# Kernel tuning notes

Hardware: AMD Instinct MI355X
Metric: run time of the kernel (lower is better)

## Reference

```python
import jax, jax.numpy as jnp
import numpy as np

NX, NQ, NU, NY = 256, 64, 8, 4
N = 65536
EPS = 0.01
STD = 0.5


def setup_inputs() -> dict:
    key = jax.random.key(0)
    ks = jax.random.split(key, 8)
    return {
        "x": jax.random.normal(ks[0], (N, NX), jnp.float32),
        "u": jax.random.normal(ks[1], (N, NU), jnp.float32),
        "X": jax.random.normal(ks[2], (NX + NQ, NX + NQ), jnp.float32) * STD,
        "U": jax.random.normal(ks[3], (NX, NQ), jnp.float32) * STD,
        "Y1": jax.random.normal(ks[4], (NX, NX), jnp.float32) * STD,
        "XP": jax.random.normal(ks[5], (NX, NX), jnp.float32) * STD,
        "B2": jax.random.normal(ks[6], (NX, NU), jnp.float32) * STD,
        "D12": jax.random.normal(ks[7], (NQ, NU), jnp.float32) * STD,
        "bv": jnp.zeros((NQ,), jnp.float32),
        "t": 0,
    }


def _constrained(X, U, Y1, XP):
    # updateParameters(): build A, B1, C1, D11 from unconstrained params.
    P = XP @ XP.T + EPS * jnp.eye(NX, dtype=XP.dtype)
    H = X @ X.T + EPS * jnp.eye(NX + NQ, dtype=X.dtype)
    H11, H12, H22 = H[:NX, :NX], H[:NX, NX:], H[NX:, NX:]
    Y = -0.5 * (H11 + Y1 - Y1.T)
    Pinv = jnp.linalg.inv(P)
    A = Pinv @ Y                                   # [nx, nx]
    lam = 0.5 * jnp.diagonal(H22)                  # Lambda diagonal
    D11 = -jnp.tril(H22, -1) / lam[:, None]        # strictly lower triangular [nq, nq]
    C1 = U.T / lam[:, None]                        # [nq, nx]
    B1 = Pinv @ (-H12 - U)                         # [nx, nq]
    return A, B1, C1, D11


def _calc_w(base, D11):
    # Forward substitution: w_i = relu(base_i + sum_{j<i} D11[i,j] * w_j).
    # D11 is strictly lower triangular and unfilled w columns are zero, so a
    # full matvec against the carry is exact.
    nq = base.shape[1]

    def step(w, inp):
        i, row, b_col = inp                        # row: [nq], b_col: [Nbatch]
        wi = jax.nn.relu(b_col + w @ row)
        return w.at[:, i].set(wi), None

    w0 = jnp.zeros_like(base)
    w, _ = jax.lax.scan(step, w0, (jnp.arange(nq), D11, base.T))
    return w


def reference(x, u, X, U, Y1, XP, B2, D12, bv, t):
    A, B1, C1, D11 = _constrained(X, U, Y1, XP)
    base = x @ C1.T + u @ D12.T + bv               # [N, nq]
    w = _calc_w(base, D11)
    x_dot = x @ A.T + w @ B1.T + u @ B2.T          # [N, nx]
    return x_dot
```

## Files before the change

### kernel.cpp

```cpp
#include <hip/hip_runtime.h>

#define EPS_C 0.01f

typedef __attribute__((ext_vector_type(8))) short short8;
typedef __attribute__((ext_vector_type(4))) float f32x4;
typedef __attribute__((ext_vector_type(4))) unsigned short u16x4;
typedef __attribute__((ext_vector_type(8))) unsigned short u16x8;

#define WS_H    0
#define WS_C    102400
#define WS_C2   167936
#define WS_Y    233472
#define WS_RHS  299008
#define WS_D11  331776
#define WS_WFH  419840
#define WS_WFM  464896
#define WS_WFL  509952
#define WS_BBH  555008
#define WS_BBM  564224
#define WS_BBL  573440
#define WS_WG   582656
#define WS_E    4776960

__device__ __forceinline__ unsigned short f2bf(float f) {
    unsigned int u = __float_as_uint(f);
    unsigned int r = (u + 0x7fffu + ((u >> 16) & 1u)) >> 16;
    return (unsigned short)r;
}
__device__ __forceinline__ float bf2f(unsigned short h) {
    return __uint_as_float(((unsigned int)h) << 16);
}
__device__ __forceinline__ void split1(float f, unsigned short& h, unsigned short& m, unsigned short& l) {
    h = f2bf(f);
    float r1 = f - bf2f(h);
    m = f2bf(r1);
    l = f2bf(r1 - bf2f(m));
}
__device__ __forceinline__ void split8(const float* v, short8& h8, short8& m8, short8& l8) {
#pragma unroll
    for (int j = 0; j < 8; ++j) {
        unsigned short h, m, l;
        split1(v[j], h, m, l);
        h8[j] = (short)h; m8[j] = (short)m; l8[j] = (short)l;
    }
}

__global__ void k_build(const float* __restrict__ Xm, const float* __restrict__ XPm,
                        float* __restrict__ H, float* __restrict__ P) {
    int idx = blockIdx.x * 256 + threadIdx.x;
    if (idx < 102400) {
        int i = idx / 320, j = idx - i * 320;
        const float4* a = (const float4*)(Xm + i * 320);
        const float4* b = (const float4*)(Xm + j * 320);
        float s = 0.f;
        for (int k = 0; k < 80; ++k) {
            float4 va = a[k], vb = b[k];
            s += va.x * vb.x + va.y * vb.y + va.z * vb.z + va.w * vb.w;
        }
        H[idx] = (i == j) ? s + EPS_C : s;
    } else {
        idx -= 102400;
        if (idx < 65536) {
            int i = idx >> 8, j = idx & 255;
            const float4* a = (const float4*)(XPm + i * 256);
            const float4* b = (const float4*)(XPm + j * 256);
            float s = 0.f;
            for (int k = 0; k < 64; ++k) {
                float4 va = a[k], vb = b[k];
                s += va.x * vb.x + va.y * vb.y + va.z * vb.z + va.w * vb.w;
            }
            P[idx] = (i == j) ? s + EPS_C : s;
        }
    }
}

__global__ void k_derived(const float* __restrict__ H, const float* __restrict__ Um,
                          const float* __restrict__ Y1, const float* __restrict__ B2,
                          const float* __restrict__ D12,
                          float* __restrict__ Y, float* __restrict__ RHS,
                          float* __restrict__ D11g,
                          unsigned short* __restrict__ Bh, unsigned short* __restrict__ Bm,
                          unsigned short* __restrict__ Bl,
                          unsigned short* __restrict__ Bbh, unsigned short* __restrict__ Bbm,
                          unsigned short* __restrict__ Bbl) {
    int idx = blockIdx.x * 256 + threadIdx.x;
    if (idx < 65536) {
        int i = idx >> 8, j = idx & 255;
        Y[idx] = -0.5f * (H[i * 320 + j] + Y1[i * 256 + j] - Y1[j * 256 + i]);
        return;
    }
    idx -= 65536;
    if (idx < 16384) {
        RHS[idx] = -H[(idx >> 6) * 320 + 256 + (idx & 63)] - Um[idx];
        return;
    }
    idx -= 16384;
    if (idx < 4096) {
        int q = idx >> 6, j = idx & 63;
        float lam = 0.5f * H[(256 + q) * 320 + 256 + q];
        D11g[idx] = (j < q) ? -H[(256 + q) * 320 + 256 + j] / lam : 0.f;
        return;
    }
    idx -= 4096;
    if (idx < 8192) {
        int o = idx >> 5, cc = idx & 31;
        float f = (cc < 8) ? B2[o * 8 + cc] : 0.f;
        unsigned short h, m, l;
        split1(f, h, m, l);
        size_t off = (size_t)o * 352 + 256 + cc;
        Bh[off] = h; Bm[off] = m; Bl[off] = l;
        return;
    }
    idx -= 8192;
    if (idx < 18432) {
        int q = idx / 288, k = idx - q * 288;
        float f;
        if (k < 256) {
            float lam = 0.5f * H[(256 + q) * 320 + 256 + q];
            f = Um[(size_t)k * 64 + q] / lam;
        } else if (k < 264) f = D12[(size_t)q * 8 + (k - 256)];
        else f = 0.f;
        unsigned short h, m, l;
        split1(f, h, m, l);
        Bbh[idx] = h; Bbm[idx] = m; Bbl[idx] = l;
    }
}

__global__ void __launch_bounds__(256) k_inv8(const float* __restrict__ Cold, float* __restrict__ E, int b) {
    __shared__ __align__(16) float M[64 * 68];
    __shared__ __align__(16) float Rs[8 * 68];
    __shared__ __align__(16) float Ts[64 * 8];
    __shared__ float E8s[8 * 9];
    const int tid = threadIdx.x;
    const int ti = tid & 15, tj = tid >> 4;
#pragma unroll
    for (int t = 0; t < 4; ++t) {
        int e = tid + t * 256;
        int r = e >> 4, c4 = e & 15;
        float4 v = *(const float4*)&Cold[(size_t)(b * 64 + r) * 256 + b * 64 + c4 * 4];
        *(float4*)&M[r * 68 + c4 * 4] = v;
    }
    __syncthreads();
    for (int s = 0; s < 8; ++s) {
        if (tid < 64) {
            const int lane = tid;
            float e8[8];
#pragma unroll
            for (int j = 0; j < 8; ++j) e8[j] = 0.f;
            if (lane < 8) {
#pragma unroll
                for (int j = 0; j < 8; ++j) e8[j] = M[(s * 8 + lane) * 68 + s * 8 + j];
            }
#pragma unroll
            for (int k = 0; k < 8; ++k) {
                const float p = __shfl(e8[k], k);
                const float rinv = 1.0f / p;
                const float f = -e8[k] * rinv;
                const bool isk = (lane == k);
#pragma unroll
                for (int j = 0; j < 8; ++j) {
                    const float prj = __shfl(e8[j], k);
                    if (j == k) e8[j] = isk ? rinv : f;
                    else        e8[j] = isk ? prj * rinv : fmaf(f, prj, e8[j]);
                }
            }
            if (lane < 8) {
#pragma unroll
                for (int j = 0; j < 8; ++j) E8s[lane * 9 + j] = e8[j];
            }
        }
        __syncthreads();
#pragma unroll
        for (int t = 0; t < 2; ++t) {
            int e = tid + t * 256;
            int r = e >> 6, c = e & 63;
            Rs[r * 68 + c] = M[(s * 8 + r) * 68 + c];
        }
#pragma unroll
        for (int t = 0; t < 2; ++t) {
            int e = tid + t * 256;
            int i = e >> 3, c = e & 7;
            float acc = 0.f;
#pragma unroll
            for (int j = 0; j < 8; ++j) acc = fmaf(M[i * 68 + s * 8 + j], E8s[j * 9 + c], acc);
            Ts[i * 8 + c] = acc;
        }
        __syncthreads();
        {
            const bool rowIn = ((ti >> 1) == s);
            const bool colIn = ((tj >> 1) == s);
            const int i0 = ti * 4, j0 = tj * 4;
            float nv[4][4];
            if (rowIn && colIn) {
#pragma unroll
                for (int r = 0; r < 4; ++r)
#pragma unroll
                    for (int d = 0; d < 4; ++d)
                        nv[r][d] = E8s[(i0 - s * 8 + r) * 9 + (j0 - s * 8 + d)];
            } else if (rowIn) {
#pragma unroll
                for (int r = 0; r < 4; ++r)
#pragma unroll
                    for (int d = 0; d < 4; ++d) {
                        float acc = 0.f;
#pragma unroll
                        for (int c = 0; c < 8; ++c)
                            acc = fmaf(E8s[(i0 - s * 8 + r) * 9 + c], Rs[c * 68 + j0 + d], acc);
                        nv[r][d] = acc;
                    }
            } else if (colIn) {
#pragma unroll
                for (int r = 0; r < 4; ++r)
#pragma unroll
                    for (int d = 0; d < 4; ++d)
                        nv[r][d] = -Ts[(i0 + r) * 8 + (j0 - s * 8 + d)];
            } else {
#pragma unroll
                for (int r = 0; r < 4; ++r)
#pragma unroll
                    for (int d = 0; d < 4; ++d) {
                        float acc = M[(i0 + r) * 68 + j0 + d];
#pragma unroll
                        for (int c = 0; c < 8; ++c)
                            acc = fmaf(-Ts[(i0 + r) * 8 + c], Rs[c * 68 + j0 + d], acc);
                        nv[r][d] = acc;
                    }
            }
#pragma unroll
            for (int r = 0; r < 4; ++r)
#pragma unroll
                for (int d = 0; d < 4; ++d) M[(i0 + r) * 68 + j0 + d] = nv[r][d];
        }
        __syncthreads();
    }
#pragma unroll
    for (int t = 0; t < 4; ++t) {
        int e = tid + t * 256;
        int r = e >> 4, c4 = e & 15;
        float4 v = *(const float4*)&M[r * 68 + c4 * 4];
        *(float4*)&E[(size_t)r * 64 + c4 * 4] = v;
    }
}

__global__ void __launch_bounds__(256) k_gjS(const float* __restrict__ Cold, float* __restrict__ Cnew,
                                             float* __restrict__ E, int b, int nb) {
    const int I = blockIdx.x >> 2, J = blockIdx.x & 3;
    const int tid = threadIdx.x;
    const int ti = tid & 15, tj = tid >> 4;
    if (I == b && J == b) {
        const int r = tid >> 2, seg = tid & 3;
#pragma unroll
        for (int t = 0; t < 4; ++t) {
            float4 v = *(const float4*)&E[(size_t)r * 64 + seg * 16 + t * 4];
            *(float4*)&Cnew[(size_t)(b * 64 + r) * 256 + b * 64 + seg * 16 + t * 4] = v;
        }
        return;
    }
    __shared__ __align__(16) float Es[64 * 68];
    __shared__ __align__(16) float S1[64 * 68];
    __shared__ __align__(16) float S2[64 * 68];
    for (int e = tid; e < 1024; e += 256) {
        int r = e >> 4, c4 = e & 15;
        float4 v = *(const float4*)&E[(size_t)r * 64 + c4 * 4];
        *(float4*)&Es[r * 68 + c4 * 4] = v;
    }
    if (I == b) {
        for (int e = tid; e < 1024; e += 256) {
            int r = e >> 4, c4 = e & 15;
            float4 v = *(const float4*)&Cold[(size_t)(b * 64 + r) * 256 + J * 64 + c4 * 4];
            *(float4*)&S1[r * 68 + c4 * 4] = v;
        }
        __syncthreads();
        float acc[4][4];
#pragma unroll
        for (int r = 0; r < 4; ++r)
#pragma unroll
            for (int d = 0; d < 4; ++d) acc[r][d] = 0.f;
        for (int mm = 0; mm < 64; ++mm) {
            float a4[4], b4[4];
#pragma unroll
            for (int d = 0; d < 4; ++d) { a4[d] = Es[(ti * 4 + d) * 68 + mm]; b4[d] = S1[mm * 68 + tj * 4 + d]; }
#pragma unroll
            for (int r = 0; r < 4; ++r)
#pragma unroll
                for (int d = 0; d < 4; ++d) acc[r][d] = fmaf(a4[r], b4[d], acc[r][d]);
        }
#pragma unroll
        for (int r = 0; r < 4; ++r) {
            float4 v = {acc[r][0], acc[r][1], acc[r][2], acc[r][3]};
            *(float4*)&Cnew[(size_t)(b * 64 + ti * 4 + r) * 256 + J * 64 + tj * 4] = v;
        }
        return;
    }
    if (J == b) {
        for (int e = tid; e < 1024; e += 256) {
            int r = e >> 4, c4 = e & 15;
            float4 v = *(const float4*)&Cold[(size_t)(I * 64 + r) * 256 + b * 64 + c4 * 4];
            *(float4*)&S1[r * 68 + c4 * 4] = v;
        }
        __syncthreads();
        float acc[4][4];
#pragma unroll
        for (int r = 0; r < 4; ++r)
#pragma unroll
            for (int d = 0; d < 4; ++d) acc[r][d] = 0.f;
        for (int kk = 0; kk < 64; ++kk) {
            float a4[4], b4[4];
#pragma unroll
            for (int d = 0; d < 4; ++d) { a4[d] = S1[(ti * 4 + d) * 68 + kk]; b4[d] = Es[kk * 68 + tj * 4 + d]; }
#pragma unroll
            for (int r = 0; r < 4; ++r)
#pragma unroll
                for (int d = 0; d < 4; ++d) acc[r][d] = fmaf(a4[r], b4[d], acc[r][d]);
        }
#pragma unroll
        for (int r = 0; r < 4; ++r) {
            float4 v = {-acc[r][0], -acc[r][1], -acc[r][2], -acc[r][3]};
            *(float4*)&Cnew[(size_t)(I * 64 + ti * 4 + r) * 256 + b * 64 + tj * 4] = v;
        }
        return;
    }
    for (int e = tid; e < 1024; e += 256) {
        int r = e >> 4, c4 = e & 15;
        float4 v = *(const float4*)&Cold[(size_t)(I * 64 + r) * 256 + b * 64 + c4 * 4];
        *(float4*)&S1[r * 68 + c4 * 4] = v;
        float4 w = *(const float4*)&Cold[(size_t)(b * 64 + r) * 256 + J * 64 + c4 * 4];
        *(float4*)&S2[r * 68 + c4 * 4] = w;
    }
    __syncthreads();
    float t4[4][4];
#pragma unroll
    for (int r = 0; r < 4; ++r)
#pragma unroll
        for (int d = 0; d < 4; ++d) t4[r][d] = 0.f;
    for (int kk = 0; kk < 64; ++kk) {
        float a4[4], b4[4];
#pragma unroll
        for (int d = 0; d < 4; ++d) { a4[d] = S1[(ti * 4 + d) * 68 + kk]; b4[d] = Es[kk * 68 + tj * 4 + d]; }
#pragma unroll
        for (int r = 0; r < 4; ++r)
#pragma unroll
            for (int d = 0; d < 4; ++d) t4[r][d] = fmaf(a4[r], b4[d], t4[r][d]);
    }
    __syncthreads();
#pragma unroll
    for (int r = 0; r < 4; ++r)
#pragma unroll
        for (int d = 0; d < 4; ++d) S1[(ti * 4 + r) * 68 + tj * 4 + d] = t4[r][d];
    __syncthreads();
    float acc[4][4];
#pragma unroll
    for (int r = 0; r < 4; ++r) {
        float4 cv = *(const float4*)&Cold[(size_t)(I * 64 + ti * 4 + r) * 256 + J * 64 + tj * 4];
        acc[r][0] = cv.x; acc[r][1] = cv.y; acc[r][2] = cv.z; acc[r][3] = cv.w;
    }
    for (int kk = 0; kk < 64; ++kk) {
        float a4[4], b4[4];
#pragma unroll
        for (int d = 0; d < 4; ++d) { a4[d] = S1[(ti * 4 + d) * 68 + kk]; b4[d] = S2[kk * 68 + tj * 4 + d]; }
#pragma unroll
        for (int r = 0; r < 4; ++r)
#pragma unroll
            for (int d = 0; d < 4; ++d) acc[r][d] = fmaf(-a4[r], b4[d], acc[r][d]);
    }
#pragma unroll
    for (int r = 0; r < 4; ++r) {
        float4 v = {acc[r][0], acc[r][1], acc[r][2], acc[r][3]};
        *(float4*)&Cnew[(size_t)(I * 64 + ti * 4 + r) * 256 + J * 64 + tj * 4] = v;
    }
    if (I == nb && J == nb) {
        float* M   = Es;
        float* Rs2 = S2;
        float* Ts2 = S2 + 1024;
        float* E8s = S2 + 1664;
        __syncthreads();
#pragma unroll
        for (int r = 0; r < 4; ++r)
#pragma unroll
            for (int d = 0; d < 4; ++d)
                M[(ti * 4 + r) * 68 + tj * 4 + d] = acc[r][d];
        __syncthreads();
        for (int s = 0; s < 8; ++s) {
            if (tid < 64) {
                const int lane = tid;
                float e8[8];
#pragma unroll
                for (int j = 0; j < 8; ++j) e8[j] = 0.f;
                if (lane < 8) {
#pragma unroll
                    for (int j = 0; j < 8; ++j) e8[j] = M[(s * 8 + lane) * 68 + s * 8 + j];
                }
#pragma unroll
                for (int k = 0; k < 8; ++k) {
                    const float p = __shfl(e8[k], k);
                    const float rinv = 1.0f / p;
                    const float f = -e8[k] * rinv;
                    const bool isk = (lane == k);
#pragma unroll
                    for (int j = 0; j < 8; ++j) {
                        const float prj = __shfl(e8[j], k);
                        if (j == k) e8[j] = isk ? rinv : f;
                        else        e8[j] = isk ? prj * rinv : fmaf(f, prj, e8[j]);
                    }
                }
                if (lane < 8) {
#pragma unroll
                    for (int j = 0; j < 8; ++j) E8s[lane * 9 + j] = e8[j];
                }
            }
            __syncthreads();
#pragma unroll
            for (int t = 0; t < 2; ++t) {
                int e = tid + t * 256;
                int r = e >> 6, c = e & 63;
                Rs2[r * 68 + c] = M[(s * 8 + r) * 68 + c];
            }
#pragma unroll
            for (int t = 0; t < 2; ++t) {
                int e = tid + t * 256;
                int i = e >> 3, c = e & 7;
                float a2 = 0.f;
#pragma unroll
                for (int j = 0; j < 8; ++j) a2 = fmaf(M[i * 68 + s * 8 + j], E8s[j * 9 + c], a2);
                Ts2[i * 8 + c] = a2;
            }
            __syncthreads();
            {
                const bool rowIn = ((ti >> 1) == s);
                const bool colIn = ((tj >> 1) == s);
                const int i0 = ti * 4, j0 = tj * 4;
                float nv[4][4];
                if (rowIn && colIn) {
#pragma unroll
                    for (int r = 0; r < 4; ++r)
#pragma unroll
                        for (int d = 0; d < 4; ++d)
                            nv[r][d] = E8s[(i0 - s * 8 + r) * 9 + (j0 - s * 8 + d)];
                } else if (rowIn) {
#pragma unroll
                    for (int r = 0; r < 4; ++r)
#pragma unroll
                        for (int d = 0; d < 4; ++d) {
                            float a2 = 0.f;
#pragma unroll
                            for (int c = 0; c < 8; ++c)
                                a2 = fmaf(E8s[(i0 - s * 8 + r) * 9 + c], Rs2[c * 68 + j0 + d], a2);
                            nv[r][d] = a2;
                        }
                } else if (colIn) {
#pragma unroll
                    for (int r = 0; r < 4; ++r)
#pragma unroll
                        for (int d = 0; d < 4; ++d)
                            nv[r][d] = -Ts2[(i0 + r) * 8 + (j0 - s * 8 + d)];
                } else {
#pragma unroll
                    for (int r = 0; r < 4; ++r)
#pragma unroll
                        for (int d = 0; d < 4; ++d) {
                            float a2 = M[(i0 + r) * 68 + j0 + d];
#pragma unroll
                            for (int c = 0; c < 8; ++c)
                                a2 = fmaf(-Ts2[(i0 + r) * 8 + c], Rs2[c * 68 + j0 + d], a2);
                            nv[r][d] = a2;
                        }
                }
#pragma unroll
                for (int r = 0; r < 4; ++r)
#pragma unroll
                    for (int d = 0; d < 4; ++d) M[(i0 + r) * 68 + j0 + d] = nv[r][d];
            }
            __syncthreads();
        }
#pragma unroll
        for (int t = 0; t < 4; ++t) {
            int e = tid + t * 256;
            int r = e >> 4, c4 = e & 15;
            float4 v = *(const float4*)&M[r * 68 + c4 * 4];
            *(float4*)&E[(size_t)r * 64 + c4 * 4] = v;
        }
    }
}

__global__ void __launch_bounds__(256) k_apply2(const float* __restrict__ PI, const float* __restrict__ Y,
                                                const float* __restrict__ RHS,
                                                unsigned short* __restrict__ Bh, unsigned short* __restrict__ Bm,
                                                unsigned short* __restrict__ Bl) {
    const int i0 = ((int)blockIdx.x / 5) * 64;
    const int c0 = ((int)blockIdx.x % 5) * 64;
    __shared__ __align__(16) float S1[64 * 68], S2[64 * 68];
    const int tid = threadIdx.x;
    const int ti = tid & 15, tj = tid >> 4;
    float acc[4][4];
#pragma unroll
    for (int r = 0; r < 4; ++r)
#pragma unroll
        for (int d = 0; d < 4; ++d) acc[r][d] = 0.f;
    for (int kc = 0; kc < 4; ++kc) {
        __syncthreads();
        for (int e = tid; e < 1024; e += 256) {
            int i = e >> 4, k4 = e & 15;
            float4 v = *(const float4*)&PI[(size_t)(i0 + i) * 256 + kc * 64 + k4 * 4];
            S1[(k4 * 4 + 0) * 68 + i] = v.x;
            S1[(k4 * 4 + 1) * 68 + i] = v.y;
            S1[(k4 * 4 + 2) * 68 + i] = v.z;
            S1[(k4 * 4 + 3) * 68 + i] = v.w;
            float4 w;
            if (c0 < 256) w = *(const float4*)&Y[(size_t)(kc * 64 + i) * 256 + c0 + k4 * 4];
            else          w = *(const float4*)&RHS[(size_t)(kc * 64 + i) * 64 + k4 * 4];
            *(float4*)&S2[i * 68 + k4 * 4] = w;
        }
        __syncthreads();
        for (int kk = 0; kk < 64; ++kk) {
            float4 pv = *(const float4*)&S1[kk * 68 + ti * 4];
            float4 gv = *(const float4*)&S2[kk * 68 + tj * 4];
            float p4[4] = {pv.x, pv.y, pv.z, pv.w};
            float g4[4] = {gv.x, gv.y, gv.z, gv.w};
#pragma unroll
            for (int r = 0; r < 4; ++r)
#pragma unroll
                for (int d = 0; d < 4; ++d) acc[r][d] = fmaf(p4[r], g4[d], acc[r][d]);
        }
    }
    const int pc0 = (c0 < 256) ? c0 : 288;
#pragma unroll
    for (int r = 0; r < 4; ++r)
#pragma unroll
        for (int d = 0; d < 4; ++d) {
            unsigned short h, m, l;
            split1(acc[r][d], h, m, l);
            size_t off = (size_t)(i0 + ti * 4 + r) * 352 + pc0 + tj * 4 + d;
            Bh[off] = h; Bm[off] = m; Bl[off] = l;
        }
}

#define XSTR 264
__global__ void __launch_bounds__(256, 3) k_base(const float* __restrict__ x, const float* __restrict__ u,
                                                 const unsigned short* __restrict__ Bbh,
                                                 const unsigned short* __restrict__ Bbm,
                                                 const unsigned short* __restrict__ Bbl,
                                                 const float* __restrict__ bv,
                                                 float* __restrict__ wg) {
    __shared__ __align__(16) unsigned short Ah[32 * XSTR];
    __shared__ __align__(16) unsigned short Am[32 * XSTR];
    __shared__ __align__(16) unsigned short Al[32 * XSTR];
    const int tid = threadIdx.x;
    const int r0 = blockIdx.x * 32;
    {
        const float4* xg4 = (const float4*)(x + (size_t)r0 * 256);
#pragma unroll
        for (int i = 0; i < 8; ++i) {
            int e = tid + i * 256, r = e >> 6, c4 = e & 63;
            float4 v = xg4[e];
            float vv[4] = {v.x, v.y, v.z, v.w};
            u16x4 hv, mv, lv;
#pragma unroll
            for (int j = 0; j < 4; ++j) {
                unsigned short h, m, l;
                split1(vv[j], h, m, l);
                hv[j] = h; mv[j] = m; lv[j] = l;
            }
            *(u16x4*)&Ah[r * XSTR + c4 * 4] = hv;
            *(u16x4*)&Am[r * XSTR + c4 * 4] = mv;
            *(u16x4*)&Al[r * XSTR + c4 * 4] = lv;
        }
    }
    __syncthreads();
    const int lane = tid & 63, wid = tid >> 6;
    const int n0 = wid * 16;
    const int lr = lane & 15, lg = lane >> 4;
    const int lk = lg * 8;
    const int noff = (n0 + lr) * 288;
    f32x4 acc[2];
    acc[0] = (f32x4){0.f, 0.f, 0.f, 0.f};
    acc[1] = (f32x4){0.f, 0.f, 0.f, 0.f};
    short8 cb_h, nb_h, b_m, b_l;
    cb_h = *(const short8*)&Bbh[noff + lk];
#pragma unroll
    for (int kt = 0; kt < 9; ++kt) {
        const int ka = kt * 32 + lk;
        b_m = *(const short8*)&Bbm[noff + ka];
        b_l = *(const short8*)&Bbl[noff + ka];
        if (kt < 8) nb_h = *(const short8*)&Bbh[noff + ka + 32];
        short8 a_h[2], a_m[2], a_l[2];
        if (kt < 8) {
            a_h[0] = *(const short8*)&Ah[lr * XSTR + ka];
            a_h[1] = *(const short8*)&Ah[(16 + lr) * XSTR + ka];
            a_m[0] = *(const short8*)&Am[lr * XSTR + ka];
            a_m[1] = *(const short8*)&Am[(16 + lr) * XSTR + ka];
            a_l[0] = *(const short8*)&Al[lr * XSTR + ka];
            a_l[1] = *(const short8*)&Al[(16 + lr) * XSTR + ka];
        } else {
            if (lg == 0) {
                float vv[8];
                const float4* up = (const float4*)&u[(size_t)(r0 + lr) * 8];
                float4 v0 = up[0], v1 = up[1];
                vv[0] = v0.x; vv[1] = v0.y; vv[2] = v0.z; vv[3] = v0.w;
                vv[4] = v1.x; vv[5] = v1.y; vv[6] = v1.z; vv[7] = v1.w;
                split8(vv, a_h[0], a_m[0], a_l[0]);
                const float4* up2 = (const float4*)&u[(size_t)(r0 + 16 + lr) * 8];
                float4 w0 = up2[0], w1 = up2[1];
                vv[0] = w0.x; vv[1] = w0.y; vv[2] = w0.z; vv[3] = w0.w;
                vv[4] = w1.x; vv[5] = w1.y; vv[6] = w1.z; vv[7] = w1.w;
                split8(vv, a_h[1], a_m[1], a_l[1]);
            } else {
                short8 z = {0, 0, 0, 0, 0, 0, 0, 0};
                a_h[0] = z; a_h[1] = z; a_m[0] = z; a_m[1] = z; a_l[0] = z; a_l[1] = z;
            }
        }
#pragma unroll
        for (int m = 0; m < 2; ++m) {
            acc[m] = __builtin_amdgcn_mfma_f32_16x16x32_bf16(a_h[m], cb_h, acc[m], 0, 0, 0);
            acc[m] = __builtin_amdgcn_mfma_f32_16x16x32_bf16(a_m[m], cb_h, acc[m], 0, 0, 0);
            acc[m] = __builtin_amdgcn_mfma_f32_16x16x32_bf16(a_l[m], cb_h, acc[m], 0, 0, 0);
        }
#pragma unroll
        for (int m = 0; m < 2; ++m) {
            acc[m] = __builtin_amdgcn_mfma_f32_16x16x32_bf16(a_h[m], b_m, acc[m], 0, 0, 0);
            acc[m] = __builtin_amdgcn_mfma_f32_16x16x32_bf16(a_m[m], b_m, acc[m], 0, 0, 0);
        }
#pragma unroll
        for (int m = 0; m < 2; ++m)
            acc[m] = __builtin_amdgcn_mfma_f32_16x16x32_bf16(a_h[m], b_l, acc[m], 0, 0, 0);
        if (kt < 8) cb_h = nb_h;
    }
    const float bvv = bv[n0 + lr];
#pragma unroll
    for (int m = 0; m < 2; ++m)
#pragma unroll
        for (int j = 0; j < 4; ++j)
            wg[(size_t)(r0 + m * 16 + lg * 4 + j) * 64 + n0 + lr] = acc[m][j] + bvv;
}

__global__ void __launch_bounds__(256) k_rec(float* __restrict__ wg, const float* __restrict__ D11g) {
    __shared__ float D[64 * 64];
    const int tid = threadIdx.x;
#pragma unroll
    for (int t = 0; t < 16; ++t) D[tid + t * 256] = D11g[tid + t * 256];
    __syncthreads();
    const size_t r = (size_t)blockIdx.x * 256 + tid;
    float w[64];
    float* wr = wg + r * 64;
#pragma unroll
    for (int c = 0; c < 16; ++c) {
        float4 v = *(const float4*)&wr[c * 4];
        w[4 * c] = v.x; w[4 * c + 1] = v.y; w[4 * c + 2] = v.z; w[4 * c + 3] = v.w;
    }
    w[0] = fmaxf(w[0], 0.f);
#pragma unroll
    for (int i = 1; i < 64; ++i) {
        float s0 = w[i], s1 = 0.f, s2 = 0.f, s3 = 0.f;
#pragma unroll
        for (int j = 0; j + 3 < i; j += 4) {
            s0 = fmaf(w[j + 0], D[i * 64 + j + 0], s0);
            s1 = fmaf(w[j + 1], D[i * 64 + j + 1], s1);
            s2 = fmaf(w[j + 2], D[i * 64 + j + 2], s2);
            s3 = fmaf(w[j + 3], D[i * 64 + j + 3], s3);
        }
#pragma unroll
        for (int j = i & ~3; j < i; ++j) s0 = fmaf(w[j], D[i * 64 + j], s0);
        w[i] = fmaxf((s0 + s1) + (s2 + s3), 0.f);
    }
#pragma unroll
    for (int c = 0; c < 16; ++c) {
        float4 v = {w[4 * c], w[4 * c + 1], w[4 * c + 2], w[4 * c + 3]};
        *(float4*)&wr[c * 4] = v;
    }
}

__global__ void __launch_bounds__(256, 3) k_m2(const float* __restrict__ x, const float* __restrict__ wg,
                                               const float* __restrict__ u,
                                               const unsigned short* __restrict__ Bh,
                                               const unsigned short* __restrict__ Bm,
                                               const unsigned short* __restrict__ Bl,
                                               float* __restrict__ out) {
    __shared__ __align__(16) unsigned short Ah[32 * XSTR];
    __shared__ __align__(16) unsigned short Am[32 * XSTR];
    __shared__ __align__(16) unsigned short Al[32 * XSTR];
    const int tid = threadIdx.x;
    const int r0 = blockIdx.x * 32;
    {
        const float4* xg4 = (const float4*)(x + (size_t)r0 * 256);
#pragma unroll
        for (int i = 0; i < 8; ++i) {
            int e = tid + i * 256, r = e >> 6, c4 = e & 63;
            float4 v = xg4[e];
            float vv[4] = {v.x, v.y, v.z, v.w};
            u16x4 hv, mv, lv;
#pragma unroll
            for (int j = 0; j < 4; ++j) {
                unsigned short h, m, l;
                split1(vv[j], h, m, l);
                hv[j] = h; mv[j] = m; lv[j] = l;
            }
            *(u16x4*)&Ah[r * XSTR + c4 * 4] = hv;
            *(u16x4*)&Am[r * XSTR + c4 * 4] = mv;
            *(u16x4*)&Al[r * XSTR + c4 * 4] = lv;
        }
    }
    __syncthreads();
    const int lane = tid & 63, wid = tid >> 6;
    const int n0 = wid * 64;
    const int lr = lane & 15, lg = lane >> 4;
    const int lk = lg * 8;
    int noff[4];
#pragma unroll
    for (int nf = 0; nf < 4; ++nf) noff[nf] = (n0 + nf * 16 + lr) * 352;
    f32x4 acc[2][4];
#pragma unroll
    for (int m = 0; m < 2; ++m)
#pragma unroll
        for (int nf = 0; nf < 4; ++nf) acc[m][nf] = (f32x4){0.f, 0.f, 0.f, 0.f};
    short8 cb_h[4], nb_h[4], b_m[4], b_l[4];
#pragma unroll
    for (int nf = 0; nf < 4; ++nf) cb_h[nf] = *(const short8*)&Bh[noff[nf] + lk];
#pragma unroll
    for (int kt = 0; kt < 11; ++kt) {
        const int ka = kt * 32 + lk;
#pragma unroll
        for (int nf = 0; nf < 4; ++nf) b_m[nf] = *(const short8*)&Bm[noff[nf] + ka];
#pragma unroll
        for (int nf = 0; nf < 4; ++nf) b_l[nf] = *(const short8*)&Bl[noff[nf] + ka];
        if (kt < 10) {
#pragma unroll
            for (int nf = 0; nf < 4; ++nf) nb_h[nf] = *(const short8*)&Bh[noff[nf] + ka + 32];
        }
        short8 a_h[2], a_m[2], a_l[2];
        if (kt < 8) {
            a_h[0] = *(const short8*)&Ah[lr * XSTR + ka];
            a_h[1] = *(const short8*)&Ah[(16 + lr) * XSTR + ka];
            a_m[0] = *(const short8*)&Am[lr * XSTR + ka];
            a_m[1] = *(const short8*)&Am[(16 + lr) * XSTR + ka];
            a_l[0] = *(const short8*)&Al[lr * XSTR + ka];
            a_l[1] = *(const short8*)&Al[(16 + lr) * XSTR + ka];
        } else if (kt == 8) {
            if (lg == 0) {
                float vv[8];
                const float4* up = (const float4*)&u[(size_t)(r0 + lr) * 8];
                float4 v0 = up[0], v1 = up[1];
                vv[0] = v0.x; vv[1] = v0.y; vv[2] = v0.z; vv[3] = v0.w;
                vv[4] = v1.x; vv[5] = v1.y; vv[6] = v1.z; vv[7] = v1.w;
                split8(vv, a_h[0], a_m[0], a_l[0]);
                const float4* up2 = (const float4*)&u[(size_t)(r0 + 16 + lr) * 8];
                float4 w0 = up2[0], w1 = up2[1];
                vv[0] = w0.x; vv[1] = w0.y; vv[2] = w0.z; vv[3] = w0.w;
                vv[4] = w1.x; vv[5] = w1.y; vv[6] = w1.z; vv[7] = w1.w;
                split8(vv, a_h[1], a_m[1], a_l[1]);
            } else {
                short8 z = {0, 0, 0, 0, 0, 0, 0, 0};
                a_h[0] = z; a_h[1] = z; a_m[0] = z; a_m[1] = z; a_l[0] = z; a_l[1] = z;
            }
        } else {
            const int wc = (kt - 9) * 32 + lk;
            float vv[8];
            const float4* wp = (const float4*)&wg[(size_t)(r0 + lr) * 64 + wc];
            float4 v0 = wp[0], v1 = wp[1];
            vv[0] = v0.x; vv[1] = v0.y; vv[2] = v0.z; vv[3] = v0.w;
            vv[4] = v1.x; vv[5] = v1.y; vv[6] = v1.z; vv[7] = v1.w;
            split8(vv, a_h[0], a_m[0], a_l[0]);
            const float4* wp2 = (const float4*)&wg[(size_t)(r0 + 16 + lr) * 64 + wc];
            float4 w0 = wp2[0], w1 = wp2[1];
            vv[0] = w0.x; vv[1] = w0.y; vv[2] = w0.z; vv[3] = w0.w;
            vv[4] = w1.x; vv[5] = w1.y; vv[6] = w1.z; vv[7] = w1.w;
            split8(vv, a_h[1], a_m[1], a_l[1]);
        }
#pragma unroll
        for (int nf = 0; nf < 4; ++nf)
#pragma unroll
            for (int m = 0; m < 2; ++m) {
                acc[m][nf] = __builtin_amdgcn_mfma_f32_16x16x32_bf16(a_h[m], cb_h[nf], acc[m][nf], 0, 0, 0);
                acc[m][nf] = __builtin_amdgcn_mfma_f32_16x16x32_bf16(a_m[m], cb_h[nf], acc[m][nf], 0, 0, 0);
                acc[m][nf] = __builtin_amdgcn_mfma_f32_16x16x32_bf16(a_l[m], cb_h[nf], acc[m][nf], 0, 0, 0);
            }
#pragma unroll
        for (int nf = 0; nf < 4; ++nf)
#pragma unroll
            for (int m = 0; m < 2; ++m) {
                acc[m][nf] = __builtin_amdgcn_mfma_f32_16x16x32_bf16(a_h[m], b_m[nf], acc[m][nf], 0, 0, 0);
                acc[m][nf] = __builtin_amdgcn_mfma_f32_16x16x32_bf16(a_m[m], b_m[nf], acc[m][nf], 0, 0, 0);
                if (kt >= 9)
                    acc[m][nf] = __builtin_amdgcn_mfma_f32_16x16x32_bf16(a_l[m], b_m[nf], acc[m][nf], 0, 0, 0);
            }
#pragma unroll
        for (int nf = 0; nf < 4; ++nf)
#pragma unroll
            for (int m = 0; m < 2; ++m) {
                acc[m][nf] = __builtin_amdgcn_mfma_f32_16x16x32_bf16(a_h[m], b_l[nf], acc[m][nf], 0, 0, 0);
                if (kt >= 9)
                    acc[m][nf] = __builtin_amdgcn_mfma_f32_16x16x32_bf16(a_m[m], b_l[nf], acc[m][nf], 0, 0, 0);
            }
        if (kt < 10) {
#pragma unroll
            for (int nf = 0; nf < 4; ++nf) cb_h[nf] = nb_h[nf];
        }
    }
#pragma unroll
    for (int m = 0; m < 2; ++m)
#pragma unroll
        for (int nf = 0; nf < 4; ++nf)
#pragma unroll
            for (int j = 0; j < 4; ++j)
                out[(size_t)(r0 + m * 16 + lg * 4 + j) * 256 + n0 + nf * 16 + lr] = acc[m][nf][j];
}

extern "C" void kernel_launch(void* const* d_in, const int* in_sizes, int n_in,
                              void* d_out, int out_size, void* d_ws, size_t ws_size,
                              hipStream_t stream) {
    const float* x   = (const float*)d_in[0];
    const float* u   = (const float*)d_in[1];
    const float* Xm  = (const float*)d_in[2];
    const float* Um  = (const float*)d_in[3];
    const float* Y1  = (const float*)d_in[4];
    const float* XPm = (const float*)d_in[5];
    const float* B2  = (const float*)d_in[6];
    const float* D12 = (const float*)d_in[7];
    const float* bv  = (const float*)d_in[8];
    float* out = (float*)d_out;
    float* ws  = (float*)d_ws;

    float* H    = ws + WS_H;
    float* C0   = ws + WS_C;
    float* C1   = ws + WS_C2;
    float* Y    = ws + WS_Y;
    float* RHS  = ws + WS_RHS;
    float* D11g = ws + WS_D11;
    float* E    = ws + WS_E;
    unsigned short* Bh  = (unsigned short*)(ws + WS_WFH);
    unsigned short* Bm  = (unsigned short*)(ws + WS_WFM);
    unsigned short* Bl  = (unsigned short*)(ws + WS_WFL);
    unsigned short* Bbh = (unsigned short*)(ws + WS_BBH);
    unsigned short* Bbm = (unsigned short*)(ws + WS_BBM);
    unsigned short* Bbl = (unsigned short*)(ws + WS_BBL);
    float* wg = ws + WS_WG;

    k_build<<<656, 256, 0, stream>>>(Xm, XPm, H, C0);
    k_derived<<<441, 256, 0, stream>>>(H, Um, Y1, B2, D12, Y, RHS, D11g,
                                       Bh, Bm, Bl, Bbh, Bbm, Bbl);
    k_base<<<2048, 256, 0, stream>>>(x, u, Bbh, Bbm, Bbl, bv, wg);
    k_rec<<<256, 256, 0, stream>>>(wg, D11g);
    k_inv8<<<1, 256, 0, stream>>>(C0, E, 0);
    k_gjS<<<16, 256, 0, stream>>>(C0, C1, E, 0, 1);
    k_gjS<<<16, 256, 0, stream>>>(C1, C0, E, 1, 2);
    k_gjS<<<16, 256, 0, stream>>>(C0, C1, E, 2, 3);
    k_gjS<<<16, 256, 0, stream>>>(C1, C0, E, 3, -1);
    k_apply2<<<20, 256, 0, stream>>>(C0, Y, RHS, Bh, Bm, Bl);
    k_m2<<<2048, 256, 0, stream>>>(x, wg, u, Bh, Bm, Bl, out);
}
```

Baseline: 373.6 us.

## Fuse base GEMM, recurrence and output GEMM into one kernel

Merges k_base, k_rec and k_m2 into a single k_main kernel. Each block keeps its 32 rows of split x in LDS and reuses them for both GEMMs, holds the base/w tile in shared memory, and runs the triangular recurrence cooperatively with 8 lanes per row and shuffle reductions. This removes the global round trip of the wg buffer, two launches, and the second load and split of x. In exchange, occupancy drops (launch bounds 3 to 2, more LDS), the B-operand prefetch pipelining is dropped, and the recurrence becomes 64 serial steps per block with only 32 of the rows active in parallel.

```diff
diff --git a/kernel.cpp b/kernel.cpp
--- a/kernel.cpp
+++ b/kernel.cpp
@@ -19,8 +19,7 @@
 #define WS_BBH  555008
 #define WS_BBM  564224
 #define WS_BBL  573440
-#define WS_WG   582656
-#define WS_E    4776960
+#define WS_E    582656
 
 __device__ __forceinline__ unsigned short f2bf(float f) {
     unsigned int u = __float_as_uint(f);
@@ -535,15 +534,21 @@
 }
 
 #define XSTR 264
-__global__ void __launch_bounds__(256, 3) k_base(const float* __restrict__ x, const float* __restrict__ u,
+__global__ void __launch_bounds__(256, 2) k_main(const float* __restrict__ x, const float* __restrict__ u,
                                                  const unsigned short* __restrict__ Bbh,
                                                  const unsigned short* __restrict__ Bbm,
                                                  const unsigned short* __restrict__ Bbl,
                                                  const float* __restrict__ bv,
-                                                 float* __restrict__ wg) {
+                                                 const float* __restrict__ D11g,
+                                                 const unsigned short* __restrict__ Bh,
+                                                 const unsigned short* __restrict__ Bm,
+                                                 const unsigned short* __restrict__ Bl,
+                                                 float* __restrict__ out) {
     __shared__ __align__(16) unsigned short Ah[32 * XSTR];
     __shared__ __align__(16) unsigned short Am[32 * XSTR];
     __shared__ __align__(16) unsigned short Al[32 * XSTR];
+    __shared__ __align__(16) float bs[32 * 68];
+    __shared__ __align__(16) float D11s[64 * 64];
     const int tid = threadIdx.x;
     const int r0 = blockIdx.x * 32;
     {
@@ -564,234 +569,191 @@
             *(u16x4*)&Am[r * XSTR + c4 * 4] = mv;
             *(u16x4*)&Al[r * XSTR + c4 * 4] = lv;
         }
+#pragma unroll
+        for (int t = 0; t < 16; ++t) D11s[tid + t * 256] = D11g[tid + t * 256];
     }
     __syncthreads();
     const int lane = tid & 63, wid = tid >> 6;
-    const int n0 = wid * 16;
     const int lr = lane & 15, lg = lane >> 4;
     const int lk = lg * 8;
-    const int noff = (n0 + lr) * 288;
-    f32x4 acc[2];
-    acc[0] = (f32x4){0.f, 0.f, 0.f, 0.f};
-    acc[1] = (f32x4){0.f, 0.f, 0.f, 0.f};
-    short8 cb_h, nb_h, b_m, b_l;
-    cb_h = *(const short8*)&Bbh[noff + lk];
-#pragma unroll
-    for (int kt = 0; kt < 9; ++kt) {
+    {
+        const int n0 = wid * 16;
+        const int noff = (n0 + lr) * 288;
+        f32x4 acc[2];
+        acc[0] = (f32x4){0.f, 0.f, 0.f, 0.f};
+        acc[1] = (f32x4){0.f, 0.f, 0.f, 0.f};
+        for (int kt = 0; kt < 9; ++kt) {
+            const int ka = kt * 32 + lk;
+            short8 a_h[2], a_m[2], a_l[2];
+            if (kt < 8) {
+                a_h[0] = *(const short8*)&Ah[lr * XSTR + ka];
+                a_h[1] = *(const short8*)&Ah[(16 + lr) * XSTR + ka];
+                a_m[0] = *(const short8*)&Am[lr * XSTR + ka];
+                a_m[1] = *(const short8*)&Am[(16 + lr) * XSTR + ka];
+                a_l[0] = *(const short8*)&Al[lr * XSTR + ka];
+                a_l[1] = *(const short8*)&Al[(16 + lr) * XSTR + ka];
+            } else {
+                if (lg == 0) {
+                    float vv[8];
+                    const float4* up = (const float4*)&u[(size_t)(r0 + lr) * 8];
+                    float4 v0 = up[0], v1 = up[1];
+                    vv[0] = v0.x; vv[1] = v0.y; vv[2] = v0.z; vv[3] = v0.w;
+                    vv[4] = v1.x; vv[5] = v1.y; vv[6] = v1.z; vv[7] = v1.w;
+                    split8(vv, a_h[0], a_m[0], a_l[0]);
+                    const float4* up2 = (const float4*)&u[(size_t)(r0 + 16 + lr) * 8];
+                    float4 w0 = up2[0], w1 = up2[1];
+                    vv[0] = w0.x; vv[1] = w0.y; vv[2] = w0.z; vv[3] = w0.w;
+                    vv[4] = w1.x; vv[5] = w1.y; vv[6] = w1.z; vv[7] = w1.w;
+                    split8(vv, a_h[1], a_m[1], a_l[1]);
+                } else {
+                    short8 z = {0, 0, 0, 0, 0, 0, 0, 0};
+                    a_h[0] = z; a_h[1] = z; a_m[0] = z; a_m[1] = z; a_l[0] = z; a_l[1] = z;
+                }
+            }
+            short8 b_h = *(const short8*)&Bbh[noff + ka];
+            short8 b_m = *(const short8*)&Bbm[noff + ka];
+            short8 b_l = *(const short8*)&Bbl[noff + ka];
+#pragma unroll
+            for (int m = 0; m < 2; ++m) {
+                acc[m] = __builtin_amdgcn_mfma_f32_16x16x32_bf16(a_h[m], b_h, acc[m], 0, 0, 0);
+                acc[m] = __builtin_amdgcn_mfma_f32_16x16x32_bf16(a_m[m], b_h, acc[m], 0, 0, 0);
+                acc[m] = __builtin_amdgcn_mfma_f32_16x16x32_bf16(a_h[m], b_m, acc[m], 0, 0, 0);
+                acc[m] = __builtin_amdgcn_mfma_f32_16x16x32_bf16(a_l[m], b_h, acc[m], 0, 0, 0);
+                acc[m] = __builtin_amdgcn_mfma_f32_16x16x32_bf16(a_m[m], b_m, acc[m], 0, 0, 0);
+                acc[m] = __builtin_amdgcn_mfma_f32_16x16x32_bf16(a_h[m], b_l, acc[m], 0, 0, 0);
+            }
+        }
+        const float bvv = bv[n0 + lr];
+#pragma unroll
+        for (int m = 0; m < 2; ++m)
+#pragma unroll
+            for (int j = 0; j < 4; ++j)
+                bs[(m * 16 + lg * 4 + j) * 68 + n0 + lr] = acc[m][j] + bvv;
+    }
+    __syncthreads();
+    {
+        const int p = tid & 7, rr = tid >> 3;
+        float* wrow = bs + rr * 68;
+        for (int i = 0; i < 64; ++i) {
+            float s = 0.f;
+            for (int j = p; j < i; j += 8) s = fmaf(wrow[j], D11s[i * 64 + j], s);
+            s += __shfl_xor(s, 1);
+            s += __shfl_xor(s, 2);
+            s += __shfl_xor(s, 4);
+            if (p == 0) {
+                const float wi = wrow[i] + s;
+                wrow[i] = wi > 0.f ? wi : 0.f;
+            }
+        }
+    }
+    __syncthreads();
+    const int n0 = wid * 64;
+    f32x4 acc[2][4];
+#pragma unroll
+    for (int m = 0; m < 2; ++m)
+#pragma unroll
+        for (int nf = 0; nf < 4; ++nf) acc[m][nf] = (f32x4){0.f, 0.f, 0.f, 0.f};
+
+#define M2_MFMA6()                                                                               \
+    for (int nf = 0; nf < 4; ++nf) {                                                             \
+        for (int m = 0; m < 2; ++m) {                                                            \
+            acc[m][nf] = __builtin_amdgcn_mfma_f32_16x16x32_bf16(a_h[m], b_h[nf], acc[m][nf], 0, 0, 0); \
+            acc[m][nf] = __builtin_amdgcn_mfma_f32_16x16x32_bf16(a_m[m], b_h[nf], acc[m][nf], 0, 0, 0); \
+            acc[m][nf] = __builtin_amdgcn_mfma_f32_16x16x32_bf16(a_h[m], b_m[nf], acc[m][nf], 0, 0, 0); \
+            acc[m][nf] = __builtin_amdgcn_mfma_f32_16x16x32_bf16(a_l[m], b_h[nf], acc[m][nf], 0, 0, 0); \
+            acc[m][nf] = __builtin_amdgcn_mfma_f32_16x16x32_bf16(a_m[m], b_m[nf], acc[m][nf], 0, 0, 0); \
+            acc[m][nf] = __builtin_amdgcn_mfma_f32_16x16x32_bf16(a_h[m], b_l[nf], acc[m][nf], 0, 0, 0); \
+        }                                                                                        \
+    }
+
+    for (int kt = 0; kt < 8; ++kt) {
         const int ka = kt * 32 + lk;
-        b_m = *(const short8*)&Bbm[noff + ka];
-        b_l = *(const short8*)&Bbl[noff + ka];
-        if (kt < 8) nb_h = *(const short8*)&Bbh[noff + ka + 32];
         short8 a_h[2], a_m[2], a_l[2];
-        if (kt < 8) {
-            a_h[0] = *(const short8*)&Ah[lr * XSTR + ka];
-            a_h[1] = *(const short8*)&Ah[(16 + lr) * XSTR + ka];
-            a_m[0] = *(const short8*)&Am[lr * XSTR + ka];
-            a_m[1] = *(const short8*)&Am[(16 + lr) * XSTR + ka];
-            a_l[0] = *(const short8*)&Al[lr * XSTR + ka];
-            a_l[1] = *(const short8*)&Al[(16 + lr) * XSTR + ka];
+        a_h[0] = *(const short8*)&Ah[lr * XSTR + ka];
+        a_h[1] = *(const short8*)&Ah[(16 + lr) * XSTR + ka];
+        a_m[0] = *(const short8*)&Am[lr * XSTR + ka];
+        a_m[1] = *(const short8*)&Am[(16 + lr) * XSTR + ka];
+        a_l[0] = *(const short8*)&Al[lr * XSTR + ka];
+        a_l[1] = *(const short8*)&Al[(16 + lr) * XSTR + ka];
+        short8 b_h[4], b_m[4], b_l[4];
+#pragma unroll
+        for (int nf = 0; nf < 4; ++nf) {
+            const size_t n = (size_t)(n0 + nf * 16 + lr);
+            b_h[nf] = *(const short8*)&Bh[n * 352 + ka];
+            b_m[nf] = *(const short8*)&Bm[n * 352 + ka];
+            b_l[nf] = *(const short8*)&Bl[n * 352 + ka];
+        }
+#pragma unroll
+        M2_MFMA6()
+    }
+    {
+        const int ka = 256 + lk;
+        short8 a_h[2], a_m[2], a_l[2];
+        if (lg == 0) {
+            float vv[8];
+            const float4* up = (const float4*)&u[(size_t)(r0 + lr) * 8];
+            float4 v0 = up[0], v1 = up[1];
+            vv[0] = v0.x; vv[1] = v0.y; vv[2] = v0.z; vv[3] = v0.w;
+            vv[4] = v1.x; vv[5] = v1.y; vv[6] = v1.z; vv[7] = v1.w;
+            split8(vv, a_h[0], a_m[0], a_l[0]);
+            const float4* up2 = (const float4*)&u[(size_t)(r0 + 16 + lr) * 8];
+            float4 w0 = up2[0], w1 = up2[1];
+            vv[0] = w0.x; vv[1] = w0.y; vv[2] = w0.z; vv[3] = w0.w;
+            vv[4] = w1.x; vv[5] = w1.y; vv[6] = w1.z; vv[7] = w1.w;
+            split8(vv, a_h[1], a_m[1], a_l[1]);
         } else {
-            if (lg == 0) {
-                float vv[8];
-                const float4* up = (const float4*)&u[(size_t)(r0 + lr) * 8];
-                float4 v0 = up[0], v1 = up[1];
-                vv[0] = v0.x; vv[1] = v0.y; vv[2] = v0.z; vv[3] = v0.w;
-                vv[4] = v1.x; vv[5] = v1.y; vv[6] = v1.z; vv[7] = v1.w;
-                split8(vv, a_h[0], a_m[0], a_l[0]);
-                const float4* up2 = (const float4*)&u[(size_t)(r0 + 16 + lr) * 8];
-                float4 w0 = up2[0], w1 = up2[1];
-                vv[0] = w0.x; vv[1] = w0.y; vv[2] = w0.z; vv[3] = w0.w;
-                vv[4] = w1.x; vv[5] = w1.y; vv[6] = w1.z; vv[7] = w1.w;
-                split8(vv, a_h[1], a_m[1], a_l[1]);
-            } else {
-                short8 z = {0, 0, 0, 0, 0, 0, 0, 0};
-                a_h[0] = z; a_h[1] = z; a_m[0] = z; a_m[1] = z; a_l[0] = z; a_l[1] = z;
-            }
-        }
-#pragma unroll
-        for (int m = 0; m < 2; ++m) {
-            acc[m] = __builtin_amdgcn_mfma_f32_16x16x32_bf16(a_h[m], cb_h, acc[m], 0, 0, 0);
-            acc[m] = __builtin_amdgcn_mfma_f32_16x16x32_bf16(a_m[m], cb_h, acc[m], 0, 0, 0);
-            acc[m] = __builtin_amdgcn_mfma_f32_16x16x32_bf16(a_l[m], cb_h, acc[m], 0, 0, 0);
-        }
-#pragma unroll
-        for (int m = 0; m < 2; ++m) {
-            acc[m] = __builtin_amdgcn_mfma_f32_16x16x32_bf16(a_h[m], b_m, acc[m], 0, 0, 0);
-            acc[m] = __builtin_amdgcn_mfma_f32_16x16x32_bf16(a_m[m], b_m, acc[m], 0, 0, 0);
-        }
-#pragma unroll
-        for (int m = 0; m < 2; ++m)
-            acc[m] = __builtin_amdgcn_mfma_f32_16x16x32_bf16(a_h[m], b_l, acc[m], 0, 0, 0);
-        if (kt < 8) cb_h = nb_h;
-    }
-    const float bvv = bv[n0 + lr];
-#pragma unroll
-    for (int m = 0; m < 2; ++m)
-#pragma unroll
-        for (int j = 0; j < 4; ++j)
-            wg[(size_t)(r0 + m * 16 + lg * 4 + j) * 64 + n0 + lr] = acc[m][j] + bvv;
-}
-
-__global__ void __launch_bounds__(256) k_rec(float* __restrict__ wg, const float* __restrict__ D11g) {
-    __shared__ float D[64 * 64];
-    const int tid = threadIdx.x;
-#pragma unroll
-    for (int t = 0; t < 16; ++t) D[tid + t * 256] = D11g[tid + t * 256];
-    __syncthreads();
-    const size_t r = (size_t)blockIdx.x * 256 + tid;
-    float w[64];
-    float* wr = wg + r * 64;
-#pragma unroll
-    for (int c = 0; c < 16; ++c) {
-        float4 v = *(const float4*)&wr[c * 4];
-        w[4 * c] = v.x; w[4 * c + 1] = v.y; w[4 * c + 2] = v.z; w[4 * c + 3] = v.w;
-    }
-    w[0] = fmaxf(w[0], 0.f);
-#pragma unroll
-    for (int i = 1; i < 64; ++i) {
-        float s0 = w[i], s1 = 0.f, s2 = 0.f, s3 = 0.f;
-#pragma unroll
-        for (int j = 0; j + 3 < i; j += 4) {
-            s0 = fmaf(w[j + 0], D[i * 64 + j + 0], s0);
-            s1 = fmaf(w[j + 1], D[i * 64 + j + 1], s1);
-            s2 = fmaf(w[j + 2], D[i * 64 + j + 2], s2);
-            s3 = fmaf(w[j + 3], D[i * 64 + j + 3], s3);
-        }
-#pragma unroll
-        for (int j = i & ~3; j < i; ++j) s0 = fmaf(w[j], D[i * 64 + j], s0);
-        w[i] = fmaxf((s0 + s1) + (s2 + s3), 0.f);
-    }
-#pragma unroll
-    for (int c = 0; c < 16; ++c) {
-        float4 v = {w[4 * c], w[4 * c + 1], w[4 * c + 2], w[4 * c + 3]};
-        *(float4*)&wr[c * 4] = v;
-    }
-}
-
-__global__ void __launch_bounds__(256, 3) k_m2(const float* __restrict__ x, const float* __restrict__ wg,
-                                               const float* __restrict__ u,
-                                               const unsigned short* __restrict__ Bh,
-                                               const unsigned short* __restrict__ Bm,
-                                               const unsigned short* __restrict__ Bl,
-                                               float* __restrict__ out) {
-    __shared__ __align__(16) unsigned short Ah[32 * XSTR];
-    __shared__ __align__(16) unsigned short Am[32 * XSTR];
-    __shared__ __align__(16) unsigned short Al[32 * XSTR];
-    const int tid = threadIdx.x;
-    const int r0 = blockIdx.x * 32;
-    {
-        const float4* xg4 = (const float4*)(x + (size_t)r0 * 256);
-#pragma unroll
-        for (int i = 0; i < 8; ++i) {
-            int e = tid + i * 256, r = e >> 6, c4 = e & 63;
-            float4 v = xg4[e];
-            float vv[4] = {v.x, v.y, v.z, v.w};
-            u16x4 hv, mv, lv;
-#pragma unroll
-            for (int j = 0; j < 4; ++j) {
-                unsigned short h, m, l;
-                split1(vv[j], h, m, l);
-                hv[j] = h; mv[j] = m; lv[j] = l;
-            }
-            *(u16x4*)&Ah[r * XSTR + c4 * 4] = hv;
-            *(u16x4*)&Am[r * XSTR + c4 * 4] = mv;
-            *(u16x4*)&Al[r * XSTR + c4 * 4] = lv;
-        }
-    }
-    __syncthreads();
-    const int lane = tid & 63, wid = tid >> 6;
-    const int n0 = wid * 64;
-    const int lr = lane & 15, lg = lane >> 4;
-    const int lk = lg * 8;
-    int noff[4];
-#pragma unroll
-    for (int nf = 0; nf < 4; ++nf) noff[nf] = (n0 + nf * 16 + lr) * 352;
-    f32x4 acc[2][4];
-#pragma unroll
-    for (int m = 0; m < 2; ++m)
-#pragma unroll
-        for (int nf = 0; nf < 4; ++nf) acc[m][nf] = (f32x4){0.f, 0.f, 0.f, 0.f};
-    short8 cb_h[4], nb_h[4], b_m[4], b_l[4];
-#pragma unroll
-    for (int nf = 0; nf < 4; ++nf) cb_h[nf] = *(const short8*)&Bh[noff[nf] + lk];
-#pragma unroll
-    for (int kt = 0; kt < 11; ++kt) {
+            short8 z = {0, 0, 0, 0, 0, 0, 0, 0};
+            a_h[0] = z; a_h[1] = z; a_m[0] = z; a_m[1] = z; a_l[0] = z; a_l[1] = z;
+        }
+        short8 b_h[4], b_m[4], b_l[4];
+#pragma unroll
+        for (int nf = 0; nf < 4; ++nf) {
+            const size_t n = (size_t)(n0 + nf * 16 + lr);
+            b_h[nf] = *(const short8*)&Bh[n * 352 + ka];
+            b_m[nf] = *(const short8*)&Bm[n * 352 + ka];
+            b_l[nf] = *(const short8*)&Bl[n * 352 + ka];
+        }
+#pragma unroll
+        M2_MFMA6()
+    }
+    for (int kt = 9; kt < 11; ++kt) {
         const int ka = kt * 32 + lk;
-#pragma unroll
-        for (int nf = 0; nf < 4; ++nf) b_m[nf] = *(const short8*)&Bm[noff[nf] + ka];
-#pragma unroll
-        for (int nf = 0; nf < 4; ++nf) b_l[nf] = *(const short8*)&Bl[noff[nf] + ka];
-        if (kt < 10) {
-#pragma unroll
-            for (int nf = 0; nf < 4; ++nf) nb_h[nf] = *(const short8*)&Bh[noff[nf] + ka + 32];
-        }
+        const int wc = (kt - 9) * 32 + lk;
         short8 a_h[2], a_m[2], a_l[2];
-        if (kt < 8) {
-            a_h[0] = *(const short8*)&Ah[lr * XSTR + ka];
-            a_h[1] = *(const short8*)&Ah[(16 + lr) * XSTR + ka];
-            a_m[0] = *(const short8*)&Am[lr * XSTR + ka];
-            a_m[1] = *(const short8*)&Am[(16 + lr) * XSTR + ka];
-            a_l[0] = *(const short8*)&Al[lr * XSTR + ka];
-            a_l[1] = *(const short8*)&Al[(16 + lr) * XSTR + ka];
-        } else if (kt == 8) {
-            if (lg == 0) {
-                float vv[8];
-                const float4* up = (const float4*)&u[(size_t)(r0 + lr) * 8];
-                float4 v0 = up[0], v1 = up[1];
-                vv[0] = v0.x; vv[1] = v0.y; vv[2] = v0.z; vv[3] = v0.w;
-                vv[4] = v1.x; vv[5] = v1.y; vv[6] = v1.z; vv[7] = v1.w;
-                split8(vv, a_h[0], a_m[0], a_l[0]);
-                const float4* up2 = (const float4*)&u[(size_t)(r0 + 16 + lr) * 8];
-                float4 w0 = up2[0], w1 = up2[1];
-                vv[0] = w0.x; vv[1] = w0.y; vv[2] = w0.z; vv[3] = w0.w;
-                vv[4] = w1.x; vv[5] = w1.y; vv[6] = w1.z; vv[7] = w1.w;
-                split8(vv, a_h[1], a_m[1], a_l[1]);
-            } else {
-                short8 z = {0, 0, 0, 0, 0, 0, 0, 0};
-                a_h[0] = z; a_h[1] = z; a_m[0] = z; a_m[1] = z; a_l[0] = z; a_l[1] = z;
-            }
-        } else {
-            const int wc = (kt - 9) * 32 + lk;
+        {
             float vv[8];
-            const float4* wp = (const float4*)&wg[(size_t)(r0 + lr) * 64 + wc];
+            const float4* wp = (const float4*)&bs[lr * 68 + wc];
             float4 v0 = wp[0], v1 = wp[1];
             vv[0] = v0.x; vv[1] = v0.y; vv[2] = v0.z; vv[3] = v0.w;
             vv[4] = v1.x; vv[5] = v1.y; vv[6] = v1.z; vv[7] = v1.w;
             split8(vv, a_h[0], a_m[0], a_l[0]);
-            const float4* wp2 = (const float4*)&wg[(size_t)(r0 + 16 + lr) * 64 + wc];
+            const float4* wp2 = (const float4*)&bs[(16 + lr) * 68 + wc];
             float4 w0 = wp2[0], w1 = wp2[1];
             vv[0] = w0.x; vv[1] = w0.y; vv[2] = w0.z; vv[3] = w0.w;
             vv[4] = w1.x; vv[5] = w1.y; vv[6] = w1.z; vv[7] = w1.w;
             split8(vv, a_h[1], a_m[1], a_l[1]);
         }
-#pragma unroll
-        for (int nf = 0; nf < 4; ++nf)
+        short8 b_h[4], b_m[4], b_l[4];
+#pragma unroll
+        for (int nf = 0; nf < 4; ++nf) {
+            const size_t n = (size_t)(n0 + nf * 16 + lr);
+            b_h[nf] = *(const short8*)&Bh[n * 352 + ka];
+            b_m[nf] = *(const short8*)&Bm[n * 352 + ka];
+            b_l[nf] = *(const short8*)&Bl[n * 352 + ka];
+        }
+#pragma unroll
+        for (int nf = 0; nf < 4; ++nf) {
 #pragma unroll
             for (int m = 0; m < 2; ++m) {
-                acc[m][nf] = __builtin_amdgcn_mfma_f32_16x16x32_bf16(a_h[m], cb_h[nf], acc[m][nf], 0, 0, 0);
-                acc[m][nf] = __builtin_amdgcn_mfma_f32_16x16x32_bf16(a_m[m], cb_h[nf], acc[m][nf], 0, 0, 0);
-                acc[m][nf] = __builtin_amdgcn_mfma_f32_16x16x32_bf16(a_l[m], cb_h[nf], acc[m][nf], 0, 0, 0);
-            }
-#pragma unroll
-        for (int nf = 0; nf < 4; ++nf)
-#pragma unroll
-            for (int m = 0; m < 2; ++m) {
+                acc[m][nf] = __builtin_amdgcn_mfma_f32_16x16x32_bf16(a_h[m], b_h[nf], acc[m][nf], 0, 0, 0);
+                acc[m][nf] = __builtin_amdgcn_mfma_f32_16x16x32_bf16(a_m[m], b_h[nf], acc[m][nf], 0, 0, 0);
                 acc[m][nf] = __builtin_amdgcn_mfma_f32_16x16x32_bf16(a_h[m], b_m[nf], acc[m][nf], 0, 0, 0);
+                acc[m][nf] = __builtin_amdgcn_mfma_f32_16x16x32_bf16(a_l[m], b_h[nf], acc[m][nf], 0, 0, 0);
                 acc[m][nf] = __builtin_amdgcn_mfma_f32_16x16x32_bf16(a_m[m], b_m[nf], acc[m][nf], 0, 0, 0);
-                if (kt >= 9)
-                    acc[m][nf] = __builtin_amdgcn_mfma_f32_16x16x32_bf16(a_l[m], b_m[nf], acc[m][nf], 0, 0, 0);
-            }
-#pragma unroll
-        for (int nf = 0; nf < 4; ++nf)
-#pragma unroll
-            for (int m = 0; m < 2; ++m) {
                 acc[m][nf] = __builtin_amdgcn_mfma_f32_16x16x32_bf16(a_h[m], b_l[nf], acc[m][nf], 0, 0, 0);
-                if (kt >= 9)
-                    acc[m][nf] = __builtin_amdgcn_mfma_f32_16x16x32_bf16(a_m[m], b_l[nf], acc[m][nf], 0, 0, 0);
-            }
-        if (kt < 10) {
-#pragma unroll
-            for (int nf = 0; nf < 4; ++nf) cb_h[nf] = nb_h[nf];
+                acc[m][nf] = __builtin_amdgcn_mfma_f32_16x16x32_bf16(a_m[m], b_l[nf], acc[m][nf], 0, 0, 0);
+                acc[m][nf] = __builtin_amdgcn_mfma_f32_16x16x32_bf16(a_l[m], b_m[nf], acc[m][nf], 0, 0, 0);
+            }
         }
     }
 #pragma unroll
@@ -831,18 +793,15 @@
     unsigned short* Bbh = (unsigned short*)(ws + WS_BBH);
     unsigned short* Bbm = (unsigned short*)(ws + WS_BBM);
     unsigned short* Bbl = (unsigned short*)(ws + WS_BBL);
-    float* wg = ws + WS_WG;
 
     k_build<<<656, 256, 0, stream>>>(Xm, XPm, H, C0);
     k_derived<<<441, 256, 0, stream>>>(H, Um, Y1, B2, D12, Y, RHS, D11g,
                                        Bh, Bm, Bl, Bbh, Bbm, Bbl);
-    k_base<<<2048, 256, 0, stream>>>(x, u, Bbh, Bbm, Bbl, bv, wg);
-    k_rec<<<256, 256, 0, stream>>>(wg, D11g);
     k_inv8<<<1, 256, 0, stream>>>(C0, E, 0);
     k_gjS<<<16, 256, 0, stream>>>(C0, C1, E, 0, 1);
     k_gjS<<<16, 256, 0, stream>>>(C1, C0, E, 1, 2);
     k_gjS<<<16, 256, 0, stream>>>(C0, C1, E, 2, 3);
     k_gjS<<<16, 256, 0, stream>>>(C1, C0, E, 3, -1);
     k_apply2<<<20, 256, 0, stream>>>(C0, Y, RHS, Bh, Bm, Bl);
-    k_m2<<<2048, 256, 0, stream>>>(x, wg, u, Bh, Bm, Bl, out);
-}
+    k_main<<<2048, 256, 0, stream>>>(x, u, Bbh, Bbm, Bbl, bv, D11g, Bh, Bm, Bl, out);
+}
```

Result: slower. 413.4 us (+10.6%).
